# Kernel optimization log

Measured on AMD Instinct MI355X. Metric: run time of the kernel, lower is better.

The kernel has to match this reference:

```python
import jax, jax.numpy as jnp
import numpy as np

N_LVL = 127  # 8-bit symmetric: levels in [-128, 127]
BN_EPS = 1e-5


def ste_round(x):
    # straight-through estimator round (HAWQ uses STE for quantization)
    return x + jax.lax.stop_gradient(jnp.round(x) - x)


def quant_act(x):
    # symmetric per-tensor 8-bit activation quantization (QuantAct)
    s = jax.lax.stop_gradient(jnp.max(jnp.abs(x))) / N_LVL
    xq = jnp.clip(ste_round(x / s), -N_LVL - 1, N_LVL) * s
    return xq, s


def q_incept_conv(x, a_sf, w, g, b, m, v, stride, pad):
    # QuantBnConv2d: fold BN into conv, per-out-channel symmetric int8 weights
    std = jnp.sqrt(v + BN_EPS)
    wf = w * (g / std)[:, None, None, None]          # folded weight [O,I,kh,kw]
    bf = b - g * m / std                              # folded bias  [O]
    w_sf = jax.lax.stop_gradient(jnp.max(jnp.abs(wf), axis=(1, 2, 3))) / N_LVL
    wq = jnp.clip(ste_round(wf / w_sf[:, None, None, None]), -N_LVL - 1, N_LVL) * w_sf[:, None, None, None]
    conv_sf = a_sf * w_sf                             # per-channel output scale
    bq = ste_round(bf / conv_sf) * conv_sf            # bias quantized to conv scale
    y = jax.lax.conv_general_dilated(
        x, wq, window_strides=(stride, stride), padding=pad,
        dimension_numbers=('NCHW', 'OIHW', 'NCHW'))
    y = jax.nn.relu(y + bq[None, :, None, None])
    return quant_act(y)  # requantize activation (QuantAct with pre-scale)


def setup_inputs() -> dict:
    key = jax.random.key(0)
    ks = jax.random.split(key, 32)
    d = {}
    d['x'] = jax.random.normal(ks[0], (64, 384, 17, 17), jnp.float32)
    shapes = {
        'w1': (448, 384, 1, 1), 'w2': (384, 448, 3, 3),
        'w3': (384, 384, 1, 3), 'w4': (384, 384, 3, 1),
    }
    chans = {'1': 448, '2': 384, '3': 384, '4': 384}
    i = 1
    for idx in ['1', '2', '3', '4']:
        c = chans[idx]
        d['w' + idx] = jax.random.normal(ks[i], shapes['w' + idx], jnp.float32) * 0.05; i += 1
        d['g' + idx] = jax.random.uniform(ks[i], (c,), jnp.float32, 0.5, 1.5); i += 1
        d['b' + idx] = jax.random.normal(ks[i], (c,), jnp.float32) * 0.1; i += 1
        d['m' + idx] = jax.random.normal(ks[i], (c,), jnp.float32) * 0.1; i += 1
        d['v' + idx] = jax.random.uniform(ks[i], (c,), jnp.float32, 0.5, 1.5); i += 1
    return d


def reference(x, w1, g1, b1, m1, v1, w2, g2, b2, m2, v2,
              w3, g3, b3, m3, v3, w4, g4, b4, m4, v4):
    # q_input_act
    x, a_sf = quant_act(x)
    # conv_list: conv1 (1x1, 384->448), conv2 (3x3, 448->384, pad 1)
    x, a_sf = q_incept_conv(x, a_sf, w1, g1, b1, m1, v1, 1, [(0, 0), (0, 0)])
    x, a_sf = q_incept_conv(x, a_sf, w2, g2, b2, m2, v2, 1, [(1, 1), (1, 1)])
    # parallel branches
    y1, s1 = q_incept_conv(x, a_sf, w3, g3, b3, m3, v3, 1, [(0, 0), (1, 1)])  # 1x3
    y2, s2 = q_incept_conv(x, a_sf, w4, g4, b4, m4, v4, 1, [(1, 1), (0, 0)])  # 3x1
    # concat + rescaling requant (q_rescaling_activ): both branches already
    # dequantized floats; requantize to a single common scale
    cat = jnp.concatenate([y1, y2], axis=1)  # [N, 768, H, W]
    out, _ = quant_act(cat)
    return out
```

## Files before the change

### kernel.cpp

```cpp
#include <hip/hip_runtime.h>
#include <stdint.h>

#define NLVL 127.0f
#define NPOS (64 * 289)

typedef int v4i __attribute__((ext_vector_type(4)));
typedef int v16i __attribute__((ext_vector_type(16)));
typedef unsigned int uint;

__device__ __forceinline__ int swz_wg(int bid, int nwg) {
    const int q = nwg >> 3, r = nwg & 7;
    const int xcd = bid & 7;
    const int base = xcd < r ? xcd * (q + 1) : r * (q + 1) + (xcd - r) * q;
    return base + (bid >> 3);
}

__global__ __launch_bounds__(256) void amax_abs_kernel(const float* __restrict__ x,
                                                       int n, float* __restrict__ slot) {
    __shared__ float red[256];
    float lm = 0.f;
    for (int i = blockIdx.x * 256 + threadIdx.x; i < n; i += gridDim.x * 256)
        lm = fmaxf(lm, fabsf(x[i]));
    red[threadIdx.x] = lm;
    __syncthreads();
    for (int s = 128; s > 0; s >>= 1) {
        if (threadIdx.x < s) red[threadIdx.x] = fmaxf(red[threadIdx.x], red[threadIdx.x + s]);
        __syncthreads();
    }
    if (threadIdx.x == 0) atomicMax((unsigned int*)slot, __float_as_uint(red[0]));
}

__global__ __launch_bounds__(256) void quant_x_kernel(const float* __restrict__ x,
                                                      signed char* __restrict__ n0,
                                                      const float* __restrict__ scal) {
    __shared__ uint t32[64][97];
    const float s = scal[0] / NLVL;
    const int tid = threadIdx.x;
    const int pi = tid & 63;
    const int pos = blockIdx.x * 64 + pi;
    const int n = pos / 289;
    const int hw = pos - n * 289;
    const float* xb = x + (size_t)n * 384 * 289 + hw;
    for (int cq = tid >> 6; cq < 96; cq += 4) {
        uint pk = 0;
#pragma unroll
        for (int k = 0; k < 4; ++k) {
            const float f = xb[(size_t)(cq * 4 + k) * 289];
            float q = rintf(f / s);
            q = fminf(fmaxf(q, -128.f), 127.f);
            pk |= ((uint)((int)q & 0xff)) << (8 * k);
        }
        t32[pi][cq] = pk;
    }
    __syncthreads();
    for (int k = 0; k < 6; ++k) {
        const int c16 = (tid >> 6) + k * 4;
        uint4 v;
        v.x = t32[pi][c16 * 4 + 0];
        v.y = t32[pi][c16 * 4 + 1];
        v.z = t32[pi][c16 * 4 + 2];
        v.w = t32[pi][c16 * 4 + 3];
        *(uint4*)&n0[((size_t)c16 * NPOS + pos) * 16] = v;
    }
}

__global__ __launch_bounds__(256) void prep_w_kernel(
    const float* __restrict__ w, const float* __restrict__ g, const float* __restrict__ b,
    const float* __restrict__ m, const float* __restrict__ v,
    const float* __restrict__ scal, int amax_idx,
    signed char* __restrict__ wstg, float* __restrict__ conv_sf, int* __restrict__ bqi,
    int I, int KHW, int OCP, int GPT) {
    const int o = blockIdx.x;
    const int E = I * KHW;
    __shared__ float red[256];
    const float std_ = sqrtf(v[o] + 1e-5f);
    const float fac = g[o] / std_;
    float lm = 0.f;
    for (int e = threadIdx.x; e < E; e += 256)
        lm = fmaxf(lm, fabsf(w[(size_t)o * E + e] * fac));
    red[threadIdx.x] = lm;
    __syncthreads();
    for (int s = 128; s > 0; s >>= 1) {
        if (threadIdx.x < s) red[threadIdx.x] = fmaxf(red[threadIdx.x], red[threadIdx.x + s]);
        __syncthreads();
    }
    const float w_sf = red[0] / NLVL;
    for (int e = threadIdx.x; e < E; e += 256) {
        const float wf = w[(size_t)o * E + e] * fac;
        float q = rintf(wf / w_sf);
        q = fminf(fmaxf(q, -128.f), 127.f);
        const int i = e / KHW;
        const int r = e - i * KHW;
        wstg[((size_t)(r * GPT + (i >> 4)) * OCP + o) * 16 + (i & 15)] = (signed char)q;
    }
    if (threadIdx.x == 0) {
        const float a_sf = scal[amax_idx] / NLVL;
        const float csf = a_sf * w_sf;
        conv_sf[o] = csf;
        const float bf = b[o] - g[o] * m[o] / std_;
        bqi[o] = (int)rintf(bf / csf);
    }
}

template <int CINP, int COUT, int OCP, int KH, int KW, int PH, int PW>
__global__ __launch_bounds__(256) void qconv_mfma(
    const signed char* __restrict__ xin, const signed char* __restrict__ wstg,
    const float* __restrict__ conv_sf, const int* __restrict__ bqv,
    float* __restrict__ yout, float* __restrict__ amax_slot,
    const signed char* __restrict__ zero16, int coff16) {
    constexpr int KCN = CINP / 64;
    constexpr int GPT = CINP / 16;
    constexpr int NKT = KH * KW * KCN;
    static_assert(NKT % 3 == 0, "depth-3 rotation needs NKT % 3 == 0");
    constexpr int NOC = OCP / 128;
    constexpr int NPB = 145;
    __shared__ float red[256];

    const int tid = threadIdx.x;
    const int lane = tid & 63;
    const int wid = tid >> 6;
    const int l31 = lane & 31;
    const int lh = lane >> 5;

    const int wgid = swz_wg(blockIdx.x, NPB * NOC);
    const int pb = wgid / NOC;
    const int ob = wgid - pb * NOC;
    const int p_blk = pb * 128;
    const int oc_blk = ob * 128;

    int pn[2], ph_[2], pw_[2];
    bool prowok[2];
#pragma unroll
    for (int it = 0; it < 2; ++it) {
        const int myp = p_blk + (wid >> 1) * 64 + it * 32 + l31;
        prowok[it] = myp < NPOS;
        const int pc = prowok[it] ? myp : 0;
        pn[it] = pc / 289;
        const int hw = pc - pn[it] * 289;
        ph_[it] = hw / 17;
        pw_[it] = hw - ph_[it] * 17;
    }
    const int oc_col0 = oc_blk + (wid & 1) * 64 + l31;

    auto loadA = [&](int kt, v4i (&a)[2][2]) {
        const int tap = kt / KCN;
        const int kc = kt - tap * KCN;
        const int kh = tap / KW;
        const int kw = tap - kh * KW;
#pragma unroll
        for (int it = 0; it < 2; ++it) {
            const int ih = ph_[it] + kh - PH;
            const int iw = pw_[it] + kw - PW;
            const bool ok = prowok[it] & ((unsigned)ih < 17u) & ((unsigned)iw < 17u);
            const int spos = pn[it] * 289 + ih * 17 + iw;
#pragma unroll
            for (int ks = 0; ks < 2; ++ks) {
                const signed char* p =
                    ok ? xin + ((size_t)((kc * 4 + ks * 2 + lh) * NPOS + spos)) * 16 : zero16;
                a[ks][it] = *(const v4i*)p;
            }
        }
    };
    auto loadB = [&](int kt, v4i (&b)[2][2]) {
        const int tap = kt / KCN;
        const int kc = kt - tap * KCN;
        const signed char* base =
            wstg + ((size_t)(tap * GPT + kc * 4 + lh) * OCP + oc_col0) * 16;
        b[0][0] = *(const v4i*)(base);
        b[0][1] = *(const v4i*)(base + 32 * 16);
        b[1][0] = *(const v4i*)(base + (size_t)2 * OCP * 16);
        b[1][1] = *(const v4i*)(base + (size_t)2 * OCP * 16 + 32 * 16);
    };

    v16i acc[2][2] = {};

    auto compute = [&](const v4i (&a)[2][2], const v4i (&b)[2][2]) {
#pragma unroll
        for (int ks = 0; ks < 2; ++ks) {
            acc[0][0] = __builtin_amdgcn_mfma_i32_32x32x32_i8(a[ks][0], b[ks][0], acc[0][0], 0, 0, 0);
            acc[0][1] = __builtin_amdgcn_mfma_i32_32x32x32_i8(a[ks][0], b[ks][1], acc[0][1], 0, 0, 0);
            acc[1][0] = __builtin_amdgcn_mfma_i32_32x32x32_i8(a[ks][1], b[ks][0], acc[1][0], 0, 0, 0);
            acc[1][1] = __builtin_amdgcn_mfma_i32_32x32x32_i8(a[ks][1], b[ks][1], acc[1][1], 0, 0, 0);
        }
    };

    v4i aA[2][2], bA[2][2], aB[2][2], bB[2][2], aC[2][2], bC[2][2];
    loadA(0, aA); loadB(0, bA);
    loadA(1, aB); loadB(1, bB);
    loadA(2, aC); loadB(2, bC);
    for (int kt = 0; kt < NKT; kt += 3) {
        compute(aA, bA);
        if (kt + 3 < NKT) { loadA(kt + 3, aA); loadB(kt + 3, bA); }
        compute(aB, bB);
        if (kt + 4 < NKT) { loadA(kt + 4, aB); loadB(kt + 4, bB); }
        compute(aC, bC);
        if (kt + 5 < NKT) { loadA(kt + 5, aC); loadB(kt + 5, bC); }
    }

    float csf[2];
    int bb[2], ocv[2];
#pragma unroll
    for (int jt = 0; jt < 2; ++jt) {
        const int oc = oc_blk + (wid & 1) * 64 + jt * 32 + l31;
        ocv[jt] = oc;
        const bool real = oc < COUT;
        csf[jt] = real ? conv_sf[oc] : 0.f;
        bb[jt] = real ? bqv[oc] : 0;
    }
    float lm = 0.f;
#pragma unroll
    for (int it = 0; it < 2; ++it) {
#pragma unroll
        for (int reg = 0; reg < 16; ++reg) {
            const int prow_o =
                p_blk + (wid >> 1) * 64 + it * 32 + (reg & 3) + 8 * (reg >> 2) + 4 * lh;
            const bool pok = prow_o < NPOS;
#pragma unroll
            for (int jt = 0; jt < 2; ++jt) {
                int t2 = acc[it][jt][reg] + bb[jt];
                t2 = t2 > 0 ? t2 : 0;
                const float v2 = csf[jt] * (float)t2;
                if (pok && ocv[jt] < COUT) {
                    lm = fmaxf(lm, v2);
                    yout[((size_t)(coff16 + (ocv[jt] >> 4)) * NPOS + prow_o) * 16 +
                         (ocv[jt] & 15)] = v2;
                }
            }
        }
    }
    red[tid] = lm;
    __syncthreads();
    for (int s = 128; s > 0; s >>= 1) {
        if (tid < s) red[tid] = fmaxf(red[tid], red[tid + s]);
        __syncthreads();
    }
    if (tid == 0) atomicMax((unsigned int*)amax_slot, __float_as_uint(red[0]));
}

__global__ __launch_bounds__(256) void requant_kernel(const float* __restrict__ f,
                                                      signed char* __restrict__ q,
                                                      const float* __restrict__ scal,
                                                      int idx, int nvec) {
    const float s = scal[idx] / NLVL;
    for (int i = blockIdx.x * 256 + threadIdx.x; i < nvec; i += gridDim.x * 256) {
        const float4 v = ((const float4*)f)[i];
        const int b0 = (int)fminf(fmaxf(rintf(v.x / s), -128.f), 127.f);
        const int b1 = (int)fminf(fmaxf(rintf(v.y / s), -128.f), 127.f);
        const int b2 = (int)fminf(fmaxf(rintf(v.z / s), -128.f), 127.f);
        const int b3 = (int)fminf(fmaxf(rintf(v.w / s), -128.f), 127.f);
        ((unsigned int*)q)[i] =
            (b0 & 0xff) | ((b1 & 0xff) << 8) | ((b2 & 0xff) << 16) | ((b3 & 0xff) << 24);
    }
}

__global__ __launch_bounds__(256) void transpose_requant_kernel(
    const float* __restrict__ f, float* __restrict__ out,
    const float* __restrict__ scal, int idx) {
    __shared__ float tile[64][65];
    const float s = scal[idx] / NLVL;
    const int tid = threadIdx.x;
    const int w = tid >> 6, l = tid & 63;
    const int pt = blockIdx.x % 289, ct = blockIdx.x / 289;
    const int pos0 = pt * 64, c0 = ct * 64;
    const int slab = ct * 4 + w;
#pragma unroll
    for (int j = 0; j < 4; ++j) {
        const int p = (l >> 2) + j * 16;
        const int co = (l & 3) * 4;
        const float4 v = *(const float4*)&f[((size_t)slab * NPOS + pos0 + p) * 16 + co];
        tile[p][w * 16 + co + 0] = v.x;
        tile[p][w * 16 + co + 1] = v.y;
        tile[p][w * 16 + co + 2] = v.z;
        tile[p][w * 16 + co + 3] = v.w;
    }
    __syncthreads();
    const int pos = pos0 + l;
    const int n = pos / 289;
    const int hw = pos - n * 289;
#pragma unroll
    for (int k = 0; k < 16; ++k) {
        const int c = c0 + w * 16 + k;
        float v = tile[l][w * 16 + k];
        v = fminf(fmaxf(rintf(v / s), -128.f), 127.f) * s;
        out[((size_t)(n * 768 + c)) * 289 + hw] = v;
    }
}

extern "C" void kernel_launch(void* const* d_in, const int* in_sizes, int n_in,
                              void* d_out, int out_size, void* d_ws, size_t ws_size,
                              hipStream_t stream) {
    const float* x  = (const float*)d_in[0];
    const float* w1 = (const float*)d_in[1];
    const float* g1 = (const float*)d_in[2];
    const float* b1 = (const float*)d_in[3];
    const float* m1 = (const float*)d_in[4];
    const float* v1 = (const float*)d_in[5];
    const float* w2 = (const float*)d_in[6];
    const float* g2 = (const float*)d_in[7];
    const float* b2 = (const float*)d_in[8];
    const float* m2 = (const float*)d_in[9];
    const float* v2 = (const float*)d_in[10];
    const float* w3 = (const float*)d_in[11];
    const float* g3 = (const float*)d_in[12];
    const float* b3 = (const float*)d_in[13];
    const float* m3 = (const float*)d_in[14];
    const float* v3 = (const float*)d_in[15];
    const float* w4 = (const float*)d_in[16];
    const float* g4 = (const float*)d_in[17];
    const float* b4 = (const float*)d_in[18];
    const float* m4 = (const float*)d_in[19];
    const float* v4 = (const float*)d_in[20];
    float* out = (float*)d_out;
    char* ws = (char*)d_ws;

    size_t off = 0;
    auto take = [&](size_t bytes) {
        char* p = ws + off;
        off = (off + bytes + 255) & ~(size_t)255;
        return p;
    };
    float* scal = (float*)take(64);
    const signed char* zero16 = (const signed char*)(scal + 8);
    signed char* wstg1 = (signed char*)take((size_t)24 * 512 * 16);
    float* sf1 = (float*)take(448 * 4);
    int* bq1 = (int*)take(448 * 4);
    signed char* wstg2 = (signed char*)take((size_t)9 * 28 * 384 * 16);
    float* sf2 = (float*)take(384 * 4);
    int* bq2 = (int*)take(384 * 4);
    signed char* wstg3 = (signed char*)take((size_t)3 * 24 * 384 * 16);
    float* sf3 = (float*)take(384 * 4);
    int* bq3 = (int*)take(384 * 4);
    signed char* wstg4 = (signed char*)take((size_t)3 * 24 * 384 * 16);
    float* sf4 = (float*)take(384 * 4);
    int* bq4 = (int*)take(384 * 4);
    signed char* n0 = (signed char*)take((size_t)24 * NPOS * 16);
    signed char* q1 = (signed char*)take((size_t)28 * NPOS * 16);
    signed char* q2 = (signed char*)take((size_t)24 * NPOS * 16);
    float* fbuf = (float*)take((size_t)48 * NPOS * 16 * 4);

    hipMemsetAsync(scal, 0, 64, stream);
    hipMemsetAsync(wstg1, 0, (size_t)24 * 512 * 16, stream);

    amax_abs_kernel<<<1024, 256, 0, stream>>>(x, 64 * 384 * 289, scal + 0);
    quant_x_kernel<<<289, 256, 0, stream>>>(x, n0, scal);

    prep_w_kernel<<<448, 256, 0, stream>>>(w1, g1, b1, m1, v1, scal, 0, wstg1, sf1, bq1,
                                           384, 1, 512, 24);
    qconv_mfma<384, 448, 512, 1, 1, 0, 0>
        <<<145 * 4, 256, 0, stream>>>(n0, wstg1, sf1, bq1, fbuf, scal + 1, zero16, 0);
    requant_kernel<<<2048, 256, 0, stream>>>(fbuf, q1, scal, 1, 28 * NPOS * 16 / 4);

    prep_w_kernel<<<384, 256, 0, stream>>>(w2, g2, b2, m2, v2, scal, 1, wstg2, sf2, bq2,
                                           448, 9, 384, 28);
    qconv_mfma<448, 384, 384, 3, 3, 1, 1>
        <<<145 * 3, 256, 0, stream>>>(q1, wstg2, sf2, bq2, fbuf, scal + 2, zero16, 0);
    requant_kernel<<<2048, 256, 0, stream>>>(fbuf, q2, scal, 2, 24 * NPOS * 16 / 4);

    prep_w_kernel<<<384, 256, 0, stream>>>(w3, g3, b3, m3, v3, scal, 2, wstg3, sf3, bq3,
                                           384, 3, 384, 24);
    prep_w_kernel<<<384, 256, 0, stream>>>(w4, g4, b4, m4, v4, scal, 2, wstg4, sf4, bq4,
                                           384, 3, 384, 24);
    qconv_mfma<384, 384, 384, 1, 3, 0, 1>
        <<<145 * 3, 256, 0, stream>>>(q2, wstg3, sf3, bq3, fbuf, scal + 3, zero16, 0);
    qconv_mfma<384, 384, 384, 3, 1, 1, 0>
        <<<145 * 3, 256, 0, stream>>>(q2, wstg4, sf4, bq4, fbuf, scal + 3, zero16, 24);

    transpose_requant_kernel<<<289 * 12, 256, 0, stream>>>(fbuf, out, scal, 3);
}
```

Baseline: 241.1 us.

## Batch weight prep into one kernel, fuse parallel branch convs, split MFMA accumulators

All four weight-quantization passes move into a single launch at the start, which no longer depends on activation scales. Conv-scale and bias quantization are deferred into each conv epilogue, which reads the activation scale directly. The 1x3 and 3x1 branch convolutions are fused into one kernel sharing a tile schedule. The MFMA loop changes from a depth-3 register rotation to depth-2 double buffering with separate even/odd accumulators to break dependency chains. This raises register pressure, and the fused dual kernel issues its loads without a prefetch pipeline.

```diff
diff --git a/kernel.cpp b/kernel.cpp
--- a/kernel.cpp
+++ b/kernel.cpp
@@ -64,13 +64,37 @@
     }
 }
 
-__global__ __launch_bounds__(256) void prep_w_kernel(
-    const float* __restrict__ w, const float* __restrict__ g, const float* __restrict__ b,
-    const float* __restrict__ m, const float* __restrict__ v,
-    const float* __restrict__ scal, int amax_idx,
-    signed char* __restrict__ wstg, float* __restrict__ conv_sf, int* __restrict__ bqi,
-    int I, int KHW, int OCP, int GPT) {
-    const int o = blockIdx.x;
+__global__ __launch_bounds__(256) void wq_kernel(
+    const float* __restrict__ w1, const float* __restrict__ g1, const float* __restrict__ b1,
+    const float* __restrict__ m1, const float* __restrict__ v1, signed char* __restrict__ s1w,
+    float* __restrict__ s1sf, float* __restrict__ s1bf,
+    const float* __restrict__ w2, const float* __restrict__ g2, const float* __restrict__ b2,
+    const float* __restrict__ m2, const float* __restrict__ v2, signed char* __restrict__ s2w,
+    float* __restrict__ s2sf, float* __restrict__ s2bf,
+    const float* __restrict__ w3, const float* __restrict__ g3, const float* __restrict__ b3,
+    const float* __restrict__ m3, const float* __restrict__ v3, signed char* __restrict__ s3w,
+    float* __restrict__ s3sf, float* __restrict__ s3bf,
+    const float* __restrict__ w4, const float* __restrict__ g4, const float* __restrict__ b4,
+    const float* __restrict__ m4, const float* __restrict__ v4, signed char* __restrict__ s4w,
+    float* __restrict__ s4sf, float* __restrict__ s4bf) {
+    const int bid = blockIdx.x;
+    const float *w, *g, *b, *m, *v;
+    signed char* wstg;
+    float *wsf, *bfv;
+    int I, KHW, OCP, GPT, o;
+    if (bid < 448) {
+        w = w1; g = g1; b = b1; m = m1; v = v1; wstg = s1w; wsf = s1sf; bfv = s1bf;
+        I = 384; KHW = 1; OCP = 512; GPT = 24; o = bid;
+    } else if (bid < 832) {
+        w = w2; g = g2; b = b2; m = m2; v = v2; wstg = s2w; wsf = s2sf; bfv = s2bf;
+        I = 448; KHW = 9; OCP = 384; GPT = 28; o = bid - 448;
+    } else if (bid < 1216) {
+        w = w3; g = g3; b = b3; m = m3; v = v3; wstg = s3w; wsf = s3sf; bfv = s3bf;
+        I = 384; KHW = 3; OCP = 384; GPT = 24; o = bid - 832;
+    } else {
+        w = w4; g = g4; b = b4; m = m4; v = v4; wstg = s4w; wsf = s4sf; bfv = s4bf;
+        I = 384; KHW = 3; OCP = 384; GPT = 24; o = bid - 1216;
+    }
     const int E = I * KHW;
     __shared__ float red[256];
     const float std_ = sqrtf(v[o] + 1e-5f);
@@ -94,24 +118,21 @@
         wstg[((size_t)(r * GPT + (i >> 4)) * OCP + o) * 16 + (i & 15)] = (signed char)q;
     }
     if (threadIdx.x == 0) {
-        const float a_sf = scal[amax_idx] / NLVL;
-        const float csf = a_sf * w_sf;
-        conv_sf[o] = csf;
-        const float bf = b[o] - g[o] * m[o] / std_;
-        bqi[o] = (int)rintf(bf / csf);
+        wsf[o] = w_sf;
+        bfv[o] = b[o] - g[o] * m[o] / std_;
     }
 }
 
 template <int CINP, int COUT, int OCP, int KH, int KW, int PH, int PW>
 __global__ __launch_bounds__(256) void qconv_mfma(
     const signed char* __restrict__ xin, const signed char* __restrict__ wstg,
-    const float* __restrict__ conv_sf, const int* __restrict__ bqv,
+    const float* __restrict__ wsf, const float* __restrict__ bfv,
+    const float* __restrict__ scal, int sidx,
     float* __restrict__ yout, float* __restrict__ amax_slot,
     const signed char* __restrict__ zero16, int coff16) {
     constexpr int KCN = CINP / 64;
     constexpr int GPT = CINP / 16;
     constexpr int NKT = KH * KW * KCN;
-    static_assert(NKT % 3 == 0, "depth-3 rotation needs NKT % 3 == 0");
     constexpr int NOC = OCP / 128;
     constexpr int NPB = 145;
     __shared__ float red[256];
@@ -172,31 +193,38 @@
         b[1][1] = *(const v4i*)(base + (size_t)2 * OCP * 16 + 32 * 16);
     };
 
-    v16i acc[2][2] = {};
+    v16i accE[2][2] = {}, accO[2][2] = {};
 
     auto compute = [&](const v4i (&a)[2][2], const v4i (&b)[2][2]) {
-#pragma unroll
-        for (int ks = 0; ks < 2; ++ks) {
-            acc[0][0] = __builtin_amdgcn_mfma_i32_32x32x32_i8(a[ks][0], b[ks][0], acc[0][0], 0, 0, 0);
-            acc[0][1] = __builtin_amdgcn_mfma_i32_32x32x32_i8(a[ks][0], b[ks][1], acc[0][1], 0, 0, 0);
-            acc[1][0] = __builtin_amdgcn_mfma_i32_32x32x32_i8(a[ks][1], b[ks][0], acc[1][0], 0, 0, 0);
-            acc[1][1] = __builtin_amdgcn_mfma_i32_32x32x32_i8(a[ks][1], b[ks][1], acc[1][1], 0, 0, 0);
-        }
-    };
-
-    v4i aA[2][2], bA[2][2], aB[2][2], bB[2][2], aC[2][2], bC[2][2];
-    loadA(0, aA); loadB(0, bA);
-    loadA(1, aB); loadB(1, bB);
-    loadA(2, aC); loadB(2, bC);
-    for (int kt = 0; kt < NKT; kt += 3) {
+        accE[0][0] = __builtin_amdgcn_mfma_i32_32x32x32_i8(a[0][0], b[0][0], accE[0][0], 0, 0, 0);
+        accE[0][1] = __builtin_amdgcn_mfma_i32_32x32x32_i8(a[0][0], b[0][1], accE[0][1], 0, 0, 0);
+        accE[1][0] = __builtin_amdgcn_mfma_i32_32x32x32_i8(a[0][1], b[0][0], accE[1][0], 0, 0, 0);
+        accE[1][1] = __builtin_amdgcn_mfma_i32_32x32x32_i8(a[0][1], b[0][1], accE[1][1], 0, 0, 0);
+        accO[0][0] = __builtin_amdgcn_mfma_i32_32x32x32_i8(a[1][0], b[1][0], accO[0][0], 0, 0, 0);
+        accO[0][1] = __builtin_amdgcn_mfma_i32_32x32x32_i8(a[1][0], b[1][1], accO[0][1], 0, 0, 0);
+        accO[1][0] = __builtin_amdgcn_mfma_i32_32x32x32_i8(a[1][1], b[1][0], accO[1][0], 0, 0, 0);
+        accO[1][1] = __builtin_amdgcn_mfma_i32_32x32x32_i8(a[1][1], b[1][1], accO[1][1], 0, 0, 0);
+    };
+
+    v4i aA[2][2], bA[2][2], aB[2][2], bB[2][2];
+    loadA(0, aA);
+    loadB(0, bA);
+    for (int kt = 0; kt < NKT; kt += 2) {
+        if (kt + 1 < NKT) {
+            loadA(kt + 1, aB);
+            loadB(kt + 1, bB);
+        }
         compute(aA, bA);
-        if (kt + 3 < NKT) { loadA(kt + 3, aA); loadB(kt + 3, bA); }
-        compute(aB, bB);
-        if (kt + 4 < NKT) { loadA(kt + 4, aB); loadB(kt + 4, bB); }
-        compute(aC, bC);
-        if (kt + 5 < NKT) { loadA(kt + 5, aC); loadB(kt + 5, bC); }
-    }
-
+        if (kt + 1 < NKT) {
+            if (kt + 2 < NKT) {
+                loadA(kt + 2, aA);
+                loadB(kt + 2, bA);
+            }
+            compute(aB, bB);
+        }
+    }
+
+    const float a_sf = scal[sidx] / NLVL;
     float csf[2];
     int bb[2], ocv[2];
 #pragma unroll
@@ -204,8 +232,9 @@
         const int oc = oc_blk + (wid & 1) * 64 + jt * 32 + l31;
         ocv[jt] = oc;
         const bool real = oc < COUT;
-        csf[jt] = real ? conv_sf[oc] : 0.f;
-        bb[jt] = real ? bqv[oc] : 0;
+        const float wsfv = real ? wsf[oc] : 0.f;
+        csf[jt] = a_sf * wsfv;
+        bb[jt] = real ? (int)rintf(bfv[oc] / csf[jt]) : 0;
     }
     float lm = 0.f;
 #pragma unroll
@@ -217,13 +246,149 @@
             const bool pok = prow_o < NPOS;
 #pragma unroll
             for (int jt = 0; jt < 2; ++jt) {
-                int t2 = acc[it][jt][reg] + bb[jt];
+                int t2 = accE[it][jt][reg] + accO[it][jt][reg] + bb[jt];
                 t2 = t2 > 0 ? t2 : 0;
                 const float v2 = csf[jt] * (float)t2;
                 if (pok && ocv[jt] < COUT) {
                     lm = fmaxf(lm, v2);
                     yout[((size_t)(coff16 + (ocv[jt] >> 4)) * NPOS + prow_o) * 16 +
                          (ocv[jt] & 15)] = v2;
+                }
+            }
+        }
+    }
+    red[tid] = lm;
+    __syncthreads();
+    for (int s = 128; s > 0; s >>= 1) {
+        if (tid < s) red[tid] = fmaxf(red[tid], red[tid + s]);
+        __syncthreads();
+    }
+    if (tid == 0) atomicMax((unsigned int*)amax_slot, __float_as_uint(red[0]));
+}
+
+__global__ __launch_bounds__(256) void qconv_dual(
+    const signed char* __restrict__ xin, const signed char* __restrict__ wstg3,
+    const signed char* __restrict__ wstg4,
+    const float* __restrict__ wsf3, const float* __restrict__ bf3,
+    const float* __restrict__ wsf4, const float* __restrict__ bf4,
+    const float* __restrict__ scal, int sidx,
+    float* __restrict__ yout, float* __restrict__ amax_slot,
+    const signed char* __restrict__ zero16) {
+    constexpr int KCN = 6;
+    constexpr int GPT = 24;
+    constexpr int OCP = 384;
+    constexpr int NKT = 3 * KCN;
+    constexpr int NOC = 3;
+    constexpr int NPB = 145;
+    __shared__ float red[256];
+
+    const int tid = threadIdx.x;
+    const int lane = tid & 63;
+    const int wid = tid >> 6;
+    const int l31 = lane & 31;
+    const int lh = lane >> 5;
+
+    const int wgid = swz_wg(blockIdx.x, NPB * NOC);
+    const int pb = wgid / NOC;
+    const int ob = wgid - pb * NOC;
+    const int p_blk = pb * 128;
+    const int oc_blk = ob * 128;
+
+    int pn[2], ph_[2], pw_[2];
+    bool prowok[2];
+#pragma unroll
+    for (int it = 0; it < 2; ++it) {
+        const int myp = p_blk + (wid >> 1) * 64 + it * 32 + l31;
+        prowok[it] = myp < NPOS;
+        const int pc = prowok[it] ? myp : 0;
+        pn[it] = pc / 289;
+        const int hw = pc - pn[it] * 289;
+        ph_[it] = hw / 17;
+        pw_[it] = hw - ph_[it] * 17;
+    }
+    const int oc_col0 = oc_blk + (wid & 1) * 64 + l31;
+
+    auto loadA = [&](int dh, int dw, int kc, v4i (&a)[2][2]) {
+#pragma unroll
+        for (int it = 0; it < 2; ++it) {
+            const int ih = ph_[it] + dh;
+            const int iw = pw_[it] + dw;
+            const bool ok = prowok[it] & ((unsigned)ih < 17u) & ((unsigned)iw < 17u);
+            const int spos = pn[it] * 289 + ih * 17 + iw;
+#pragma unroll
+            for (int ks = 0; ks < 2; ++ks) {
+                const signed char* p =
+                    ok ? xin + ((size_t)((kc * 4 + ks * 2 + lh) * NPOS + spos)) * 16 : zero16;
+                a[ks][it] = *(const v4i*)p;
+            }
+        }
+    };
+    auto loadB = [&](const signed char* wstg, int tap, int kc, v4i (&b)[2][2]) {
+        const signed char* base =
+            wstg + ((size_t)(tap * GPT + kc * 4 + lh) * OCP + oc_col0) * 16;
+        b[0][0] = *(const v4i*)(base);
+        b[0][1] = *(const v4i*)(base + 32 * 16);
+        b[1][0] = *(const v4i*)(base + (size_t)2 * OCP * 16);
+        b[1][1] = *(const v4i*)(base + (size_t)2 * OCP * 16 + 32 * 16);
+    };
+
+    v16i acc3[2][2] = {}, acc4[2][2] = {};
+
+    auto compute = [&](v16i (&acc)[2][2], const v4i (&a)[2][2], const v4i (&b)[2][2]) {
+#pragma unroll
+        for (int ks = 0; ks < 2; ++ks) {
+            acc[0][0] = __builtin_amdgcn_mfma_i32_32x32x32_i8(a[ks][0], b[ks][0], acc[0][0], 0, 0, 0);
+            acc[0][1] = __builtin_amdgcn_mfma_i32_32x32x32_i8(a[ks][0], b[ks][1], acc[0][1], 0, 0, 0);
+            acc[1][0] = __builtin_amdgcn_mfma_i32_32x32x32_i8(a[ks][1], b[ks][0], acc[1][0], 0, 0, 0);
+            acc[1][1] = __builtin_amdgcn_mfma_i32_32x32x32_i8(a[ks][1], b[ks][1], acc[1][1], 0, 0, 0);
+        }
+    };
+
+    for (int kt = 0; kt < NKT; ++kt) {
+        const int tap = kt / KCN;
+        const int kc = kt - tap * KCN;
+        v4i a3[2][2], a4[2][2], b3[2][2], b4[2][2];
+        loadA(0, tap - 1, kc, a3);
+        loadA(tap - 1, 0, kc, a4);
+        loadB(wstg3, tap, kc, b3);
+        loadB(wstg4, tap, kc, b4);
+        compute(acc3, a3, b3);
+        compute(acc4, a4, b4);
+    }
+
+    const float a_sf = scal[sidx] / NLVL;
+    float csf3[2], csf4[2];
+    int bb3[2], bb4[2], ocv[2];
+#pragma unroll
+    for (int jt = 0; jt < 2; ++jt) {
+        const int oc = oc_blk + (wid & 1) * 64 + jt * 32 + l31;
+        ocv[jt] = oc;
+        csf3[jt] = a_sf * wsf3[oc];
+        bb3[jt] = (int)rintf(bf3[oc] / csf3[jt]);
+        csf4[jt] = a_sf * wsf4[oc];
+        bb4[jt] = (int)rintf(bf4[oc] / csf4[jt]);
+    }
+    float lm = 0.f;
+#pragma unroll
+    for (int it = 0; it < 2; ++it) {
+#pragma unroll
+        for (int reg = 0; reg < 16; ++reg) {
+            const int prow_o =
+                p_blk + (wid >> 1) * 64 + it * 32 + (reg & 3) + 8 * (reg >> 2) + 4 * lh;
+            const bool pok = prow_o < NPOS;
+#pragma unroll
+            for (int jt = 0; jt < 2; ++jt) {
+                int t3 = acc3[it][jt][reg] + bb3[jt];
+                t3 = t3 > 0 ? t3 : 0;
+                const float v3v = csf3[jt] * (float)t3;
+                int t4 = acc4[it][jt][reg] + bb4[jt];
+                t4 = t4 > 0 ? t4 : 0;
+                const float v4v = csf4[jt] * (float)t4;
+                if (pok) {
+                    lm = fmaxf(lm, fmaxf(v3v, v4v));
+                    const size_t sl = (size_t)(ocv[jt] >> 4);
+                    yout[(sl * NPOS + prow_o) * 16 + (ocv[jt] & 15)] = v3v;
+                    yout[(((size_t)24 + sl) * NPOS + prow_o) * 16 + (ocv[jt] & 15)] = v4v;
                 }
             }
         }
@@ -323,16 +488,16 @@
     const signed char* zero16 = (const signed char*)(scal + 8);
     signed char* wstg1 = (signed char*)take((size_t)24 * 512 * 16);
     float* sf1 = (float*)take(448 * 4);
-    int* bq1 = (int*)take(448 * 4);
+    float* bf1 = (float*)take(448 * 4);
     signed char* wstg2 = (signed char*)take((size_t)9 * 28 * 384 * 16);
     float* sf2 = (float*)take(384 * 4);
-    int* bq2 = (int*)take(384 * 4);
+    float* bf2 = (float*)take(384 * 4);
     signed char* wstg3 = (signed char*)take((size_t)3 * 24 * 384 * 16);
     float* sf3 = (float*)take(384 * 4);
-    int* bq3 = (int*)take(384 * 4);
+    float* bf3 = (float*)take(384 * 4);
     signed char* wstg4 = (signed char*)take((size_t)3 * 24 * 384 * 16);
     float* sf4 = (float*)take(384 * 4);
-    int* bq4 = (int*)take(384 * 4);
+    float* bf4 = (float*)take(384 * 4);
     signed char* n0 = (signed char*)take((size_t)24 * NPOS * 16);
     signed char* q1 = (signed char*)take((size_t)28 * NPOS * 16);
     signed char* q2 = (signed char*)take((size_t)24 * NPOS * 16);
@@ -341,29 +506,24 @@
     hipMemsetAsync(scal, 0, 64, stream);
     hipMemsetAsync(wstg1, 0, (size_t)24 * 512 * 16, stream);
 
+    wq_kernel<<<1600, 256, 0, stream>>>(w1, g1, b1, m1, v1, wstg1, sf1, bf1,
+                                        w2, g2, b2, m2, v2, wstg2, sf2, bf2,
+                                        w3, g3, b3, m3, v3, wstg3, sf3, bf3,
+                                        w4, g4, b4, m4, v4, wstg4, sf4, bf4);
+
     amax_abs_kernel<<<1024, 256, 0, stream>>>(x, 64 * 384 * 289, scal + 0);
     quant_x_kernel<<<289, 256, 0, stream>>>(x, n0, scal);
 
-    prep_w_kernel<<<448, 256, 0, stream>>>(w1, g1, b1, m1, v1, scal, 0, wstg1, sf1, bq1,
-                                           384, 1, 512, 24);
     qconv_mfma<384, 448, 512, 1, 1, 0, 0>
-        <<<145 * 4, 256, 0, stream>>>(n0, wstg1, sf1, bq1, fbuf, scal + 1, zero16, 0);
+        <<<145 * 4, 256, 0, stream>>>(n0, wstg1, sf1, bf1, scal, 0, fbuf, scal + 1, zero16, 0);
     requant_kernel<<<2048, 256, 0, stream>>>(fbuf, q1, scal, 1, 28 * NPOS * 16 / 4);
 
-    prep_w_kernel<<<384, 256, 0, stream>>>(w2, g2, b2, m2, v2, scal, 1, wstg2, sf2, bq2,
-                                           448, 9, 384, 28);
     qconv_mfma<448, 384, 384, 3, 3, 1, 1>
-        <<<145 * 3, 256, 0, stream>>>(q1, wstg2, sf2, bq2, fbuf, scal + 2, zero16, 0);
+        <<<145 * 3, 256, 0, stream>>>(q1, wstg2, sf2, bf2, scal, 1, fbuf, scal + 2, zero16, 0);
     requant_kernel<<<2048, 256, 0, stream>>>(fbuf, q2, scal, 2, 24 * NPOS * 16 / 4);
 
-    prep_w_kernel<<<384, 256, 0, stream>>>(w3, g3, b3, m3, v3, scal, 2, wstg3, sf3, bq3,
-                                           384, 3, 384, 24);
-    prep_w_kernel<<<384, 256, 0, stream>>>(w4, g4, b4, m4, v4, scal, 2, wstg4, sf4, bq4,
-                                           384, 3, 384, 24);
-    qconv_mfma<384, 384, 384, 1, 3, 0, 1>
-        <<<145 * 3, 256, 0, stream>>>(q2, wstg3, sf3, bq3, fbuf, scal + 3, zero16, 0);
-    qconv_mfma<384, 384, 384, 3, 1, 1, 0>
-        <<<145 * 3, 256, 0, stream>>>(q2, wstg4, sf4, bq4, fbuf, scal + 3, zero16, 24);
+    qconv_dual<<<145 * 3, 256, 0, stream>>>(q2, wstg3, wstg4, sf3, bf3, sf4, bf4,
+                                            scal, 2, fbuf, scal + 3, zero16);
 
     transpose_requant_kernel<<<289 * 12, 256, 0, stream>>>(fbuf, out, scal, 3);
 }
```

New measurement: 254.9 us. 5.7% more time.
